# Kernel optimization log

Measured on AMD Instinct MI355X. Metric: run time of the kernel, lower is better.

Reference implementation:

```python
import jax, jax.numpy as jnp
import numpy as np

B, L, H, V = 8, 512, 256, 32000
ALPHA = 0.95  # EMA coefficient from __init__
LN_EPS = 1e-5
NORM_EPS = 1e-12  # F.normalize eps


def setup_inputs() -> dict:
    key = jax.random.key(0)
    ks = jax.random.split(key, 8)
    g = lambda k, shape, scale: (jax.random.normal(k, shape, jnp.float32) * scale)
    return {
        "seq": jax.random.randint(ks[0], (B, L), 0, V),
        "embed": g(ks[1], (V, H), 0.02),
        "W1": g(ks[2], (H, 2 * H), 1.0 / np.sqrt(H)),
        "b1": jnp.zeros((2 * H,), jnp.float32),
        "W2": g(ks[3], (2 * H, H), 1.0 / np.sqrt(2 * H)),
        "b2": jnp.zeros((H,), jnp.float32),
        "gamma": jnp.ones((H,), jnp.float32),
        "beta": jnp.zeros((H,), jnp.float32),
        "Wrp": g(ks[4], (H, H), 1.0 / np.sqrt(H)),
        "brp": jnp.zeros((H,), jnp.float32),
        "Wout": g(ks[5], (H, V), 1.0 / np.sqrt(H)),
        "bout": jnp.zeros((V,), jnp.float32),
    }


def _encoder(seq, embed, W1, b1, W2, b2, gamma, beta):
    h = embed[seq]  # [B, L, H]
    ff = jnp.maximum(h @ W1 + b1, 0.0) @ W2 + b2  # Linear-ReLU-Linear
    x = h + ff
    mu = x.mean(-1, keepdims=True)
    var = ((x - mu) ** 2).mean(-1, keepdims=True)
    return (x - mu) / jnp.sqrt(var + LN_EPS) * gamma + beta  # LayerNorm


def reference(seq, embed, W1, b1, W2, b2, gamma, beta, Wrp, brp, Wout, bout):
    h = _encoder(seq, embed, W1, b1, W2, b2, gamma, beta)  # [B, L, H]
    b, l, hd = h.shape
    keys = jnp.swapaxes(h[:, :-1, :], 0, 1)  # time-major [L-1, B, H]

    def step(M, k):
        kn = k / jnp.maximum(jnp.linalg.norm(k, axis=-1, keepdims=True), NORM_EPS)
        dv = k - jnp.einsum('bij,bj->bi', M, kn)  # delta: v - M k_hat
        M = M + (1.0 - ALPHA) * jnp.einsum('bi,bj->bij', dv, kn)  # rank-1 update
        return M, None

    M0 = jnp.zeros((b, hd, hd), h.dtype)
    M, _ = jax.lax.scan(step, M0, keys)  # sequential delta-rule recurrence
    m = jnp.einsum('bij,bj->bi', M, h[:, -1, :])  # read-out with last token
    return (m @ Wrp + brp) @ Wout + bout  # [B, V]
```

## Files before the change

kernel.cpp:

```cpp
#include <hip/hip_runtime.h>

constexpr int Bz  = 8;
constexpr int Lz  = 512;
constexpr int Hz  = 256;
constexpr int H2z = 512;
constexpr int Vz  = 32000;
constexpr int Mz  = Bz * Lz;
constexpr float CF = 0.05f;
constexpr int NB  = 16;

typedef __attribute__((ext_vector_type(8))) short bfrag8;
typedef __attribute__((ext_vector_type(4))) float f32x4v;
typedef __attribute__((ext_vector_type(4))) short s4v;

static __device__ __forceinline__ short f2bf(float f) {
  unsigned u = __builtin_bit_cast(unsigned, f);
  u += 0x7fffu + ((u >> 16) & 1u);
  return (short)(u >> 16);
}

static __device__ __forceinline__ void wcvt_tile(
    const float* __restrict__ src, short* __restrict__ dst,
    int K, int N, int n0, int k0, int tid)
{
  __shared__ float tile[64][68];
  const int rr = tid >> 4, c4 = (tid & 15) << 2;
#pragma unroll
  for (int q = 0; q < 4; ++q) {
    const int kr = rr + q * 16;
    *(float4*)&tile[kr][c4] = *(const float4*)(src + (long)(k0 + kr) * N + n0 + c4);
  }
  __syncthreads();
#pragma unroll
  for (int q = 0; q < 4; ++q) {
    const int nr = rr + q * 16;
    s4v o = { f2bf(tile[c4 + 0][nr]), f2bf(tile[c4 + 1][nr]),
              f2bf(tile[c4 + 2][nr]), f2bf(tile[c4 + 3][nr]) };
    *(s4v*)(dst + (long)(n0 + nr) * K + k0 + c4) = o;
  }
}

__global__ __launch_bounds__(256) void k_wcvt2(
    const float* __restrict__ W1, const float* __restrict__ W2,
    short* __restrict__ Wt1, short* __restrict__ Wt2)
{
  const int bx = blockIdx.x, tid = threadIdx.x;
  if (bx < 32) {
    wcvt_tile(W1, Wt1, Hz, H2z, (bx & 7) * 64, (bx >> 3) * 64, tid);
  } else {
    const int b2 = bx - 32;
    wcvt_tile(W2, Wt2, H2z, Hz, (b2 & 3) * 64, (b2 >> 2) * 64, tid);
  }
}

__global__ __launch_bounds__(256) void k_mfma1(
    const int* __restrict__ seq, const float* __restrict__ embed,
    const short* __restrict__ Wt1, const float* __restrict__ b1,
    short* __restrict__ y1bf)
{
  __shared__ short As[64][32];
  __shared__ short Bs[64][32];
  const int tid = threadIdx.x;
  const int n0 = blockIdx.x * 64, m0 = blockIdx.y * 64;
  const int w = tid >> 6, l = tid & 63;
  const int srow = tid >> 2, skq = (tid & 3) << 3;
  const long abase = (long)seq[m0 + srow] * Hz;
  const f32x4v zero = {0.f, 0.f, 0.f, 0.f};
  f32x4v acc[4] = {zero, zero, zero, zero};
  for (int kc = 0; kc < Hz; kc += 32) {
    const float4 a0 = *(const float4*)(embed + abase + kc + skq);
    const float4 a1 = *(const float4*)(embed + abase + kc + skq + 4);
    const bfrag8 bvl = *(const bfrag8*)(Wt1 + (long)(n0 + srow) * Hz + kc + skq);
    __syncthreads();
    bfrag8 av = { f2bf(a0.x), f2bf(a0.y), f2bf(a0.z), f2bf(a0.w),
                  f2bf(a1.x), f2bf(a1.y), f2bf(a1.z), f2bf(a1.w) };
    *(bfrag8*)&As[srow][skq] = av;
    *(bfrag8*)&Bs[srow][skq] = bvl;
    __syncthreads();
    const bfrag8 a = *(const bfrag8*)&As[(w << 4) + (l & 15)][(l >> 4) << 3];
#pragma unroll
    for (int nn = 0; nn < 4; ++nn) {
      const bfrag8 bb = *(const bfrag8*)&Bs[(nn << 4) + (l & 15)][(l >> 4) << 3];
      acc[nn] = __builtin_amdgcn_mfma_f32_16x16x32_bf16(a, bb, acc[nn], 0, 0, 0);
    }
  }
  const int col0 = l & 15, quad = l >> 4;
#pragma unroll
  for (int nn = 0; nn < 4; ++nn) {
    const int col = n0 + (nn << 4) + col0;
    const float bias = b1[col];
#pragma unroll
    for (int i = 0; i < 4; ++i) {
      const int row = m0 + (w << 4) + (quad << 2) + i;
      y1bf[(long)row * H2z + col] = f2bf(fmaxf(acc[nn][i] + bias, 0.0f));
    }
  }
}

__global__ __launch_bounds__(256) void k_mfma2(
    const int* __restrict__ seq, const float* __restrict__ embed,
    const short* __restrict__ y1bf, const short* __restrict__ Wt2,
    const float* __restrict__ b2, float* __restrict__ x)
{
  __shared__ short As[64][32];
  __shared__ short Bs[64][32];
  const int tid = threadIdx.x;
  const int n0 = blockIdx.x * 64, m0 = blockIdx.y * 64;
  const int w = tid >> 6, l = tid & 63;
  const int srow = tid >> 2, skq = (tid & 3) << 3;
  const f32x4v zero = {0.f, 0.f, 0.f, 0.f};
  f32x4v acc[4] = {zero, zero, zero, zero};
  for (int kc = 0; kc < H2z; kc += 32) {
    __syncthreads();
    *(bfrag8*)&As[srow][skq] = *(const bfrag8*)(y1bf + (long)(m0 + srow) * H2z + kc + skq);
    *(bfrag8*)&Bs[srow][skq] = *(const bfrag8*)(Wt2 + (long)(n0 + srow) * H2z + kc + skq);
    __syncthreads();
    const bfrag8 a = *(const bfrag8*)&As[(w << 4) + (l & 15)][(l >> 4) << 3];
#pragma unroll
    for (int nn = 0; nn < 4; ++nn) {
      const bfrag8 bb = *(const bfrag8*)&Bs[(nn << 4) + (l & 15)][(l >> 4) << 3];
      acc[nn] = __builtin_amdgcn_mfma_f32_16x16x32_bf16(a, bb, acc[nn], 0, 0, 0);
    }
  }
  const int col0 = l & 15, quad = l >> 4;
#pragma unroll
  for (int i = 0; i < 4; ++i) {
    const int row = m0 + (w << 4) + (quad << 2) + i;
    const long ebase = (long)seq[row] * Hz;
#pragma unroll
    for (int nn = 0; nn < 4; ++nn) {
      const int col = n0 + (nn << 4) + col0;
      x[(long)row * Hz + col] = acc[nn][i] + b2[col] + embed[ebase + col];
    }
  }
}

__global__ __launch_bounds__(256) void k_ln(
    const float* __restrict__ x, const float* __restrict__ gamma,
    const float* __restrict__ beta, float* __restrict__ h,
    float* __restrict__ hn, short* __restrict__ Knb)
{
  const int lane = threadIdx.x & 63;
  const long row = (long)blockIdx.x * 4 + (threadIdx.x >> 6);
  const int b = (int)(row >> 9), t = (int)(row & 511);
  const int off = lane << 2;
  const float4 xv = *(const float4*)(x + row * Hz + off);
  float s  = xv.x + xv.y + xv.z + xv.w;
  float ss = xv.x * xv.x + xv.y * xv.y + xv.z * xv.z + xv.w * xv.w;
#pragma unroll
  for (int o = 32; o >= 1; o >>= 1) { s += __shfl_xor(s, o); ss += __shfl_xor(ss, o); }
  const float mu   = s * (1.0f / Hz);
  const float var  = ss * (1.0f / Hz) - mu * mu;
  const float rstd = rsqrtf(var + 1e-5f);
  const float4 gv = *(const float4*)(gamma + off);
  const float4 bv = *(const float4*)(beta + off);
  float4 hv;
  hv.x = (xv.x - mu) * rstd * gv.x + bv.x;
  hv.y = (xv.y - mu) * rstd * gv.y + bv.y;
  hv.z = (xv.z - mu) * rstd * gv.z + bv.z;
  hv.w = (xv.w - mu) * rstd * gv.w + bv.w;
  *(float4*)(h + row * Hz + off) = hv;
  float hs = hv.x * hv.x + hv.y * hv.y + hv.z * hv.z + hv.w * hv.w;
#pragma unroll
  for (int o = 32; o >= 1; o >>= 1) hs += __shfl_xor(hs, o);
  const float inv = 1.0f / fmaxf(sqrtf(hs), 1e-12f);
  float4 nv = {hv.x * inv, hv.y * inv, hv.z * inv, hv.w * inv};
  *(float4*)(hn + row * Hz + off) = nv;
  if (t < 511) {
    const int sidx = 510 - t;
    s4v o = { f2bf(nv.x), f2bf(nv.y), f2bf(nv.z), f2bf(nv.w) };
    *(s4v*)(Knb + ((long)b * 512 + sidx) * Hz + off) = o;
  } else {
    s4v z = {0, 0, 0, 0};
    *(s4v*)(Knb + ((long)b * 512 + 511) * Hz + off) = z;
  }
}

__global__ __launch_bounds__(256) void k_gramT(
    const short* __restrict__ Knb, float* __restrict__ G)
{
  const int nb = blockIdx.x, mb = blockIdx.y, b = blockIdx.z;
  if (nb > mb) return;
  __shared__ short As[64][32];
  __shared__ short Bs[64][32];
  const short* Kb = Knb + (long)b * 512 * Hz;
  const int tid = threadIdx.x;
  const int w = tid >> 6, l = tid & 63;
  const int srow = tid >> 2, skq = (tid & 3) << 3;
  const f32x4v zero = {0.f, 0.f, 0.f, 0.f};
  f32x4v acc[4] = {zero, zero, zero, zero};
  for (int kc = 0; kc < Hz; kc += 32) {
    __syncthreads();
    *(bfrag8*)&As[srow][skq] = *(const bfrag8*)(Kb + (long)(mb * 64 + srow) * Hz + kc + skq);
    *(bfrag8*)&Bs[srow][skq] = *(const bfrag8*)(Kb + (long)(nb * 64 + srow) * Hz + kc + skq);
    __syncthreads();
    const bfrag8 a = *(const bfrag8*)&As[(w << 4) + (l & 15)][(l >> 4) << 3];
#pragma unroll
    for (int nn = 0; nn < 4; ++nn) {
      const bfrag8 bb = *(const bfrag8*)&Bs[(nn << 4) + (l & 15)][(l >> 4) << 3];
      acc[nn] = __builtin_amdgcn_mfma_f32_16x16x32_bf16(a, bb, acc[nn], 0, 0, 0);
    }
  }
  const int col0 = l & 15, quad = l >> 4;
  float* Gb = G + (long)b * 512 * 512;
#pragma unroll
  for (int nn = 0; nn < 4; ++nn) {
    const int col = nb * 64 + (nn << 4) + col0;
#pragma unroll
    for (int i = 0; i < 4; ++i) {
      const int row = mb * 64 + (w << 4) + (quad << 2) + i;
      Gb[(long)row * 512 + col] = acc[nn][i];
    }
  }
}

__global__ __launch_bounds__(256) void k_winv(
    const float* __restrict__ G, float* __restrict__ Wsol)
{
  __shared__ float Gs[32][33];
  __shared__ float Ws[32][33];
  __shared__ float part[8][33];
  const int blk = blockIdx.x, b = blockIdx.y;
  const int tid = threadIdx.x;
  const float* Gb = G + (long)b * 512 * 512;
  const int s0 = blk << 5;
  {
    const int i = tid >> 3, j4 = (tid & 7) << 2;
    *(float4*)&Gs[i][j4] = *(const float4*)(Gb + (long)(s0 + i) * 512 + s0 + j4);
    const float4 z = {0.f, 0.f, 0.f, 0.f};
    *(float4*)&Ws[i][j4] = z;
  }
  __syncthreads();
  if (tid == 0) Ws[0][0] = 1.0f;
  __syncthreads();
  const int c = tid & 31, g = tid >> 5;
  for (int i = 1; i < 32; ++i) {
    float partial = 0.0f;
#pragma unroll
    for (int q = 0; q < 4; ++q) {
      const int j = g + (q << 3);
      if (j < i) partial = fmaf(Gs[i][j], Ws[j][c], partial);
    }
    part[g][c] = partial;
    __syncthreads();
    if (tid < 32) {
      const float sum = part[0][c] + part[1][c] + part[2][c] + part[3][c] +
                        part[4][c] + part[5][c] + part[6][c] + part[7][c];
      Ws[i][c] = ((i == c) ? 1.0f : 0.0f) - CF * sum;
    }
    __syncthreads();
  }
  {
    const int i = tid >> 3, j4 = (tid & 7) << 2;
    float* dst = Wsol + ((long)(b * NB + blk) << 10);
    *(float4*)(dst + i * 32 + j4) = *(const float4*)&Ws[i][j4];
  }
}

__global__ __launch_bounds__(256) void k_p(
    const float* __restrict__ h, const float* __restrict__ hn,
    float* __restrict__ p)
{
  __shared__ float qs[Hz];
  const int b = blockIdx.y, tid = threadIdx.x;
  qs[tid] = h[((long)b * Lz + 511) * Hz + tid];
  __syncthreads();
  const int s = blockIdx.x * 16 + (tid >> 4);
  const int ch = (tid & 15) << 4;
  float acc = 0.0f;
  if (s <= 510) {
    const float* src = hn + ((long)b * Lz + (510 - s)) * Hz + ch;
#pragma unroll
    for (int q = 0; q < 4; ++q) {
      const float4 v = *(const float4*)(src + 4 * q);
      acc += v.x * qs[ch + 4 * q] + v.y * qs[ch + 4 * q + 1] +
             v.z * qs[ch + 4 * q + 2] + v.w * qs[ch + 4 * q + 3];
    }
  }
#pragma unroll
  for (int o = 8; o >= 1; o >>= 1) acc += __shfl_xor(acc, o);
  if ((tid & 15) == 0) p[(long)b * 512 + s] = acc;
}

__global__ __launch_bounds__(256) void k_solve(
    const float* __restrict__ G, const float* __restrict__ p,
    const float* __restrict__ Wsol, float* __restrict__ d_all)
{
  __shared__ float ds[512];
  __shared__ float part[32][9];
  __shared__ float rhs[32];
  const int b = blockIdx.x, tid = threadIdx.x;
  const int i = tid >> 3, g = tid & 7;
  const float* Gb = G + (long)b * 512 * 512;
  const float* pb = p + (long)b * 512;

  for (int blk = 0; blk < NB; ++blk) {
    float acc0 = 0.0f, acc1 = 0.0f;
    const float* grow = Gb + (long)(blk * 32 + i) * 512 + (g << 2);
    int bp = 0;
    for (; bp + 1 < blk; bp += 2) {
      const float4 g0 = *(const float4*)(grow + bp * 32);
      const float4 g1 = *(const float4*)(grow + bp * 32 + 32);
      const int j0 = bp * 32 + (g << 2), j1 = j0 + 32;
      acc0 += g0.x * ds[j0] + g0.y * ds[j0 + 1] + g0.z * ds[j0 + 2] + g0.w * ds[j0 + 3];
      acc1 += g1.x * ds[j1] + g1.y * ds[j1 + 1] + g1.z * ds[j1 + 2] + g1.w * ds[j1 + 3];
    }
    if (bp < blk) {
      const float4 gv = *(const float4*)(grow + bp * 32);
      const int j = bp * 32 + (g << 2);
      acc0 += gv.x * ds[j] + gv.y * ds[j + 1] + gv.z * ds[j + 2] + gv.w * ds[j + 3];
    }
    part[i][g] = acc0 + acc1;
    __syncthreads();
    if (tid < 32) {
      float c = part[tid][0] + part[tid][1] + part[tid][2] + part[tid][3] +
                part[tid][4] + part[tid][5] + part[tid][6] + part[tid][7];
      rhs[tid] = pb[blk * 32 + tid] - CF * c;
    }
    __syncthreads();
    const float* wrow = Wsol + ((long)(b * NB + blk) << 10) + i * 32 + (g << 2);
    const float4 wv = *(const float4*)wrow;
    const int k0 = g << 2;
    part[i][g] = wv.x * rhs[k0] + wv.y * rhs[k0 + 1] +
                 wv.z * rhs[k0 + 2] + wv.w * rhs[k0 + 3];
    __syncthreads();
    if (tid < 32) {
      float dv = part[tid][0] + part[tid][1] + part[tid][2] + part[tid][3] +
                 part[tid][4] + part[tid][5] + part[tid][6] + part[tid][7];
      if (blk == NB - 1 && tid == 31) dv = 0.0f;
      ds[blk * 32 + tid] = dv;
      d_all[(long)b * 512 + blk * 32 + tid] = dv;
    }
    __syncthreads();
  }
}

__global__ __launch_bounds__(256) void k_mrp(
    const float* __restrict__ h, const float* __restrict__ d_all,
    float* __restrict__ part)
{
  const int c = blockIdx.x, b = blockIdx.y, tid = threadIdx.x;
  const float* hb = h + (long)b * Lz * Hz;
  const float* db = d_all + ((long)b << 9);
  const int t0 = c * 16;
  const int t1 = (t0 + 16 < 511) ? t0 + 16 : 511;
  float acc = 0.0f;
#pragma unroll 4
  for (int t = t0; t < t1; ++t)
    acc = fmaf(db[510 - t], hb[(long)t * Hz + tid], acc);
  part[((long)b * 32 + c) * Hz + tid] = acc;
}

__global__ __launch_bounds__(256) void k_mr2(
    const float* __restrict__ part, const float* __restrict__ Wrp,
    const float* __restrict__ brp, float* __restrict__ r)
{
  __shared__ float ms[Hz];
  const int b = blockIdx.x, tid = threadIdx.x;
  float acc = 0.0f;
#pragma unroll
  for (int c = 0; c < 32; ++c) acc += part[((long)b * 32 + c) * Hz + tid];
  ms[tid] = CF * acc;
  __syncthreads();
  float racc = 0.0f;
#pragma unroll 8
  for (int e = 0; e < Hz; ++e)
    racc = fmaf(ms[e], Wrp[(long)e * Hz + tid], racc);
  r[b * Hz + tid] = racc + brp[tid];
}

__global__ __launch_bounds__(256) void k_outproj(
    const float* __restrict__ r, const float* __restrict__ Wout,
    const float* __restrict__ bout, float* __restrict__ out)
{
  __shared__ float rs[8 * Hz];
  __shared__ float part[4][8][64];
  const int tid = threadIdx.x, w = tid >> 6, lane = tid & 63;
  ((float4*)rs)[tid * 2 + 0] = ((const float4*)r)[tid * 2 + 0];
  ((float4*)rs)[tid * 2 + 1] = ((const float4*)r)[tid * 2 + 1];
  __syncthreads();
  const int col = blockIdx.x * 64 + lane;
  float acc[8] = {};
  const int i0 = w << 6;
#pragma unroll 8
  for (int ii = 0; ii < 64; ++ii) {
    const int i = i0 + ii;
    const float wv = Wout[(long)i * Vz + col];
#pragma unroll
    for (int bb = 0; bb < 8; ++bb) acc[bb] = fmaf(rs[bb * Hz + i], wv, acc[bb]);
  }
#pragma unroll
  for (int bb = 0; bb < 8; ++bb) part[w][bb][lane] = acc[bb];
  __syncthreads();
  const float bo = bout[col];
  float s0 = part[0][w][lane] + part[1][w][lane] + part[2][w][lane] + part[3][w][lane];
  out[(long)w * Vz + col] = s0 + bo;
  const int w4 = w + 4;
  float s1 = part[0][w4][lane] + part[1][w4][lane] + part[2][w4][lane] + part[3][w4][lane];
  out[(long)w4 * Vz + col] = s1 + bo;
}

extern "C" void kernel_launch(void* const* d_in, const int* in_sizes, int n_in,
                              void* d_out, int out_size, void* d_ws, size_t ws_size,
                              hipStream_t stream)
{
  const int*   seq   = (const int*)  d_in[0];
  const float* embed = (const float*)d_in[1];
  const float* W1    = (const float*)d_in[2];
  const float* b1    = (const float*)d_in[3];
  const float* W2    = (const float*)d_in[4];
  const float* b2    = (const float*)d_in[5];
  const float* gamma = (const float*)d_in[6];
  const float* beta  = (const float*)d_in[7];
  const float* Wrp   = (const float*)d_in[8];
  const float* brp   = (const float*)d_in[9];
  const float* Wout  = (const float*)d_in[10];
  const float* bout  = (const float*)d_in[11];
  float* out = (float*)d_out;

  char* ws = (char*)d_ws;
  const size_t MB = 1024u * 1024u;
  short* y1bf = (short*)(ws);
  float* xb   = (float*)(ws + 4 * MB);
  float* Gf   = (float*)(ws);
  float* hb   = (float*)(ws + 8 * MB);
  float* hnb  = (float*)(ws + 12 * MB);
  short* Knb  = (short*)(ws + 16 * MB);
  short* Wt1  = (short*)(ws + 18 * MB);
  short* Wt2  = (short*)(ws + 18 * MB + 256 * 1024);
  float* Wsol = (float*)(ws + 18 * MB + 512 * 1024);
  float* pbuf = (float*)(ws + 19 * MB);
  float* dall = (float*)(ws + 19 * MB + 16 * 1024);
  float* prt  = (float*)(ws + 19 * MB + 32 * 1024);
  float* rb   = (float*)(ws + 19 * MB + 288 * 1024);

  k_wcvt2<<<64, 256, 0, stream>>>(W1, W2, Wt1, Wt2);
  k_mfma1<<<dim3(H2z / 64, Mz / 64), 256, 0, stream>>>(seq, embed, Wt1, b1, y1bf);
  k_mfma2<<<dim3(Hz / 64, Mz / 64), 256, 0, stream>>>(seq, embed, y1bf, Wt2, b2, xb);
  k_ln<<<Mz / 4, 256, 0, stream>>>(xb, gamma, beta, hb, hnb, Knb);
  k_gramT<<<dim3(8, 8, Bz), 256, 0, stream>>>(Knb, Gf);
  k_winv<<<dim3(NB, Bz), 256, 0, stream>>>(Gf, Wsol);
  k_p<<<dim3(32, Bz), 256, 0, stream>>>(hb, hnb, pbuf);
  k_solve<<<Bz, 256, 0, stream>>>(Gf, pbuf, Wsol, dall);
  k_mrp<<<dim3(32, Bz), 256, 0, stream>>>(hb, dall, prt);
  k_mr2<<<Bz, 256, 0, stream>>>(prt, Wrp, brp, rb);
  k_outproj<<<Vz / 64, 256, 0, stream>>>(rb, Wout, bout, out);
}
```

Baseline: 205.3 us.

## Fuse diagonal-block inverse into gram kernel and merge solve tail into one kernel

The 32x32 diagonal-block triangular inverse now runs inside the gram kernel's diagonal tiles, working on the accumulator values still held there, so the separate k_winv launch and its reread of G go away. The p projection, blocked forward solve, M readout and Wrp projection are merged into a single 1024-thread per-batch kernel, with the Wsol blocks staged in shared memory. This removes five launches and their intermediate global round-trips. In exchange, the tail runs on only 8 blocks, the inverse is serial per column in registers, and the larger block means more threads wait at each barrier.

```diff
diff --git a/kernel.cpp b/kernel.cpp
--- a/kernel.cpp
+++ b/kernel.cpp
@@ -177,12 +177,14 @@
 }
 
 __global__ __launch_bounds__(256) void k_gramT(
-    const short* __restrict__ Knb, float* __restrict__ G)
+    const short* __restrict__ Knb, float* __restrict__ G,
+    float* __restrict__ Wsol)
 {
   const int nb = blockIdx.x, mb = blockIdx.y, b = blockIdx.z;
   if (nb > mb) return;
   __shared__ short As[64][32];
   __shared__ short Bs[64][32];
+  __shared__ float Gs2[2][32][33];
   const short* Kb = Knb + (long)b * 512 * Hz;
   const int tid = threadIdx.x;
   const int w = tid >> 6, l = tid & 63;
@@ -212,161 +214,135 @@
       Gb[(long)row * 512 + col] = acc[nn][i];
     }
   }
-}
-
-__global__ __launch_bounds__(256) void k_winv(
-    const float* __restrict__ G, float* __restrict__ Wsol)
-{
-  __shared__ float Gs[32][33];
-  __shared__ float Ws[32][33];
-  __shared__ float part[8][33];
-  const int blk = blockIdx.x, b = blockIdx.y;
-  const int tid = threadIdx.x;
-  const float* Gb = G + (long)b * 512 * 512;
-  const int s0 = blk << 5;
+  if (mb != nb) return;
+#pragma unroll
+  for (int nn = 0; nn < 4; ++nn) {
+    const int lc = (nn << 4) + col0;
+#pragma unroll
+    for (int i = 0; i < 4; ++i) {
+      const int lr = (w << 4) + (quad << 2) + i;
+      if ((lr >> 5) == (lc >> 5)) Gs2[lr >> 5][lr & 31][lc & 31] = acc[nn][i];
+    }
+  }
+  __syncthreads();
+  if (w < 2 && l < 32) {
+    const int c = l;
+    float wv[32];
+    wv[0] = (c == 0) ? 1.0f : 0.0f;
+#pragma unroll
+    for (int i = 1; i < 32; ++i) {
+      float sum = 0.0f;
+#pragma unroll
+      for (int j = 0; j < i; ++j) sum = fmaf(Gs2[w][i][j], wv[j], sum);
+      wv[i] = ((i == c) ? 1.0f : 0.0f) - CF * sum;
+    }
+    const int blk = mb * 2 + w;
+    float* dst = Wsol + ((long)(b * NB + blk) << 10) + c;
+#pragma unroll
+    for (int i = 0; i < 32; ++i) dst[i * 32] = wv[i];
+  }
+}
+
+__global__ __launch_bounds__(1024) void k_tail(
+    const float* __restrict__ h, const float* __restrict__ hn,
+    const float* __restrict__ G, const float* __restrict__ Wsol,
+    const float* __restrict__ Wrp, const float* __restrict__ brp,
+    float* __restrict__ r)
+{
+  __shared__ float Wl[16][32][32];
+  __shared__ float qs[256];
+  __shared__ float ps[512];
+  __shared__ float ds[512];
+  __shared__ float part[32][33];
+  __shared__ float rhs[32];
+  __shared__ float pm[4][256];
+  __shared__ float ms[256];
+  const int b = blockIdx.x, tid = threadIdx.x;
+  const float* hb  = h  + (long)b * Lz * Hz;
+  const float* hnb = hn + (long)b * Lz * Hz;
+  const float* Gb  = G + (long)b * 512 * 512;
+
+  if (tid < 256) qs[tid] = hb[511 * Hz + tid];
   {
-    const int i = tid >> 3, j4 = (tid & 7) << 2;
-    *(float4*)&Gs[i][j4] = *(const float4*)(Gb + (long)(s0 + i) * 512 + s0 + j4);
-    const float4 z = {0.f, 0.f, 0.f, 0.f};
-    *(float4*)&Ws[i][j4] = z;
-  }
-  __syncthreads();
-  if (tid == 0) Ws[0][0] = 1.0f;
-  __syncthreads();
-  const int c = tid & 31, g = tid >> 5;
-  for (int i = 1; i < 32; ++i) {
-    float partial = 0.0f;
-#pragma unroll
-    for (int q = 0; q < 4; ++q) {
-      const int j = g + (q << 3);
-      if (j < i) partial = fmaf(Gs[i][j], Ws[j][c], partial);
-    }
-    part[g][c] = partial;
+    const float4* src = (const float4*)(Wsol + ((long)(b * NB) << 10));
+    float4* dst = (float4*)&Wl[0][0][0];
+#pragma unroll
+    for (int q = 0; q < 4; ++q) dst[tid + q * 1024] = src[tid + q * 1024];
+  }
+  __syncthreads();
+
+  {
+    const int s = tid >> 1, hf = tid & 1;
+    float acc = 0.0f;
+    if (s < 511) {
+      const float* src = hnb + (long)(510 - s) * Hz + hf * 128;
+#pragma unroll
+      for (int q = 0; q < 32; ++q) {
+        const float4 v = *(const float4*)(src + 4 * q);
+        const int e = hf * 128 + 4 * q;
+        acc += v.x * qs[e] + v.y * qs[e + 1] + v.z * qs[e + 2] + v.w * qs[e + 3];
+      }
+    }
+    acc += __shfl_xor(acc, 1);
+    if (hf == 0) ps[s] = acc;
+  }
+  __syncthreads();
+
+  const int si = tid >> 5, sg = tid & 31;
+  for (int blk = 0; blk < NB; ++blk) {
+    float acc = 0.0f;
+    const float* grow = Gb + (long)(blk * 32 + si) * 512;
+    const int nq = (blk + 3) >> 2;
+    for (int q = 0; q < nq; ++q) {
+      const int c = (sg << 2) + (q << 7);
+      if (c < blk * 32) {
+        const float4 gv = *(const float4*)(grow + c);
+        acc += gv.x * ds[c] + gv.y * ds[c + 1] + gv.z * ds[c + 2] + gv.w * ds[c + 3];
+      }
+    }
+    part[si][sg] = acc;
     __syncthreads();
     if (tid < 32) {
-      const float sum = part[0][c] + part[1][c] + part[2][c] + part[3][c] +
-                        part[4][c] + part[5][c] + part[6][c] + part[7][c];
-      Ws[i][c] = ((i == c) ? 1.0f : 0.0f) - CF * sum;
-    }
-    __syncthreads();
-  }
-  {
-    const int i = tid >> 3, j4 = (tid & 7) << 2;
-    float* dst = Wsol + ((long)(b * NB + blk) << 10);
-    *(float4*)(dst + i * 32 + j4) = *(const float4*)&Ws[i][j4];
-  }
-}
-
-__global__ __launch_bounds__(256) void k_p(
-    const float* __restrict__ h, const float* __restrict__ hn,
-    float* __restrict__ p)
-{
-  __shared__ float qs[Hz];
-  const int b = blockIdx.y, tid = threadIdx.x;
-  qs[tid] = h[((long)b * Lz + 511) * Hz + tid];
-  __syncthreads();
-  const int s = blockIdx.x * 16 + (tid >> 4);
-  const int ch = (tid & 15) << 4;
-  float acc = 0.0f;
-  if (s <= 510) {
-    const float* src = hn + ((long)b * Lz + (510 - s)) * Hz + ch;
-#pragma unroll
-    for (int q = 0; q < 4; ++q) {
-      const float4 v = *(const float4*)(src + 4 * q);
-      acc += v.x * qs[ch + 4 * q] + v.y * qs[ch + 4 * q + 1] +
-             v.z * qs[ch + 4 * q + 2] + v.w * qs[ch + 4 * q + 3];
-    }
-  }
-#pragma unroll
-  for (int o = 8; o >= 1; o >>= 1) acc += __shfl_xor(acc, o);
-  if ((tid & 15) == 0) p[(long)b * 512 + s] = acc;
-}
-
-__global__ __launch_bounds__(256) void k_solve(
-    const float* __restrict__ G, const float* __restrict__ p,
-    const float* __restrict__ Wsol, float* __restrict__ d_all)
-{
-  __shared__ float ds[512];
-  __shared__ float part[32][9];
-  __shared__ float rhs[32];
-  const int b = blockIdx.x, tid = threadIdx.x;
-  const int i = tid >> 3, g = tid & 7;
-  const float* Gb = G + (long)b * 512 * 512;
-  const float* pb = p + (long)b * 512;
-
-  for (int blk = 0; blk < NB; ++blk) {
-    float acc0 = 0.0f, acc1 = 0.0f;
-    const float* grow = Gb + (long)(blk * 32 + i) * 512 + (g << 2);
-    int bp = 0;
-    for (; bp + 1 < blk; bp += 2) {
-      const float4 g0 = *(const float4*)(grow + bp * 32);
-      const float4 g1 = *(const float4*)(grow + bp * 32 + 32);
-      const int j0 = bp * 32 + (g << 2), j1 = j0 + 32;
-      acc0 += g0.x * ds[j0] + g0.y * ds[j0 + 1] + g0.z * ds[j0 + 2] + g0.w * ds[j0 + 3];
-      acc1 += g1.x * ds[j1] + g1.y * ds[j1 + 1] + g1.z * ds[j1 + 2] + g1.w * ds[j1 + 3];
-    }
-    if (bp < blk) {
-      const float4 gv = *(const float4*)(grow + bp * 32);
-      const int j = bp * 32 + (g << 2);
-      acc0 += gv.x * ds[j] + gv.y * ds[j + 1] + gv.z * ds[j + 2] + gv.w * ds[j + 3];
-    }
-    part[i][g] = acc0 + acc1;
+      float s8 = 0.0f;
+#pragma unroll
+      for (int k = 0; k < 32; ++k) s8 += part[tid][k];
+      rhs[tid] = ps[blk * 32 + tid] - CF * s8;
+    }
+    __syncthreads();
+    part[si][sg] = Wl[blk][si][sg] * rhs[sg];
     __syncthreads();
     if (tid < 32) {
-      float c = part[tid][0] + part[tid][1] + part[tid][2] + part[tid][3] +
-                part[tid][4] + part[tid][5] + part[tid][6] + part[tid][7];
-      rhs[tid] = pb[blk * 32 + tid] - CF * c;
-    }
-    __syncthreads();
-    const float* wrow = Wsol + ((long)(b * NB + blk) << 10) + i * 32 + (g << 2);
-    const float4 wv = *(const float4*)wrow;
-    const int k0 = g << 2;
-    part[i][g] = wv.x * rhs[k0] + wv.y * rhs[k0 + 1] +
-                 wv.z * rhs[k0 + 2] + wv.w * rhs[k0 + 3];
-    __syncthreads();
-    if (tid < 32) {
-      float dv = part[tid][0] + part[tid][1] + part[tid][2] + part[tid][3] +
-                 part[tid][4] + part[tid][5] + part[tid][6] + part[tid][7];
+      float dv = 0.0f;
+#pragma unroll
+      for (int k = 0; k < 32; ++k) dv += part[tid][k];
       if (blk == NB - 1 && tid == 31) dv = 0.0f;
       ds[blk * 32 + tid] = dv;
-      d_all[(long)b * 512 + blk * 32 + tid] = dv;
-    }
-    __syncthreads();
-  }
-}
-
-__global__ __launch_bounds__(256) void k_mrp(
-    const float* __restrict__ h, const float* __restrict__ d_all,
-    float* __restrict__ part)
-{
-  const int c = blockIdx.x, b = blockIdx.y, tid = threadIdx.x;
-  const float* hb = h + (long)b * Lz * Hz;
-  const float* db = d_all + ((long)b << 9);
-  const int t0 = c * 16;
-  const int t1 = (t0 + 16 < 511) ? t0 + 16 : 511;
-  float acc = 0.0f;
-#pragma unroll 4
-  for (int t = t0; t < t1; ++t)
-    acc = fmaf(db[510 - t], hb[(long)t * Hz + tid], acc);
-  part[((long)b * 32 + c) * Hz + tid] = acc;
-}
-
-__global__ __launch_bounds__(256) void k_mr2(
-    const float* __restrict__ part, const float* __restrict__ Wrp,
-    const float* __restrict__ brp, float* __restrict__ r)
-{
-  __shared__ float ms[Hz];
-  const int b = blockIdx.x, tid = threadIdx.x;
-  float acc = 0.0f;
-#pragma unroll
-  for (int c = 0; c < 32; ++c) acc += part[((long)b * 32 + c) * Hz + tid];
-  ms[tid] = CF * acc;
-  __syncthreads();
-  float racc = 0.0f;
+    }
+    __syncthreads();
+  }
+
+  {
+    const int c = tid & 255, q4 = tid >> 8;
+    float acc = 0.0f;
+    const int t0 = q4 << 7;
+    for (int t = t0; t < t0 + 128; ++t)
+      if (t < 511) acc = fmaf(ds[510 - t], hb[(long)t * Hz + c], acc);
+    pm[q4][c] = acc;
+  }
+  __syncthreads();
+  if (tid < 256) ms[tid] = CF * (pm[0][tid] + pm[1][tid] + pm[2][tid] + pm[3][tid]);
+  __syncthreads();
+  {
+    const int c = tid & 255, eq = tid >> 8;
+    float acc = 0.0f;
 #pragma unroll 8
-  for (int e = 0; e < Hz; ++e)
-    racc = fmaf(ms[e], Wrp[(long)e * Hz + tid], racc);
-  r[b * Hz + tid] = racc + brp[tid];
+    for (int e = eq * 64; e < eq * 64 + 64; ++e)
+      acc = fmaf(ms[e], Wrp[(long)e * Hz + c], acc);
+    pm[eq][c] = acc;
+  }
+  __syncthreads();
+  if (tid < 256)
+    r[b * Hz + tid] = pm[0][tid] + pm[1][tid] + pm[2][tid] + pm[3][tid] + brp[tid];
 }
 
 __global__ __launch_bounds__(256) void k_outproj(
@@ -429,20 +405,13 @@
   short* Wt1  = (short*)(ws + 18 * MB);
   short* Wt2  = (short*)(ws + 18 * MB + 256 * 1024);
   float* Wsol = (float*)(ws + 18 * MB + 512 * 1024);
-  float* pbuf = (float*)(ws + 19 * MB);
-  float* dall = (float*)(ws + 19 * MB + 16 * 1024);
-  float* prt  = (float*)(ws + 19 * MB + 32 * 1024);
-  float* rb   = (float*)(ws + 19 * MB + 288 * 1024);
+  float* rb   = (float*)(ws + 19 * MB);
 
   k_wcvt2<<<64, 256, 0, stream>>>(W1, W2, Wt1, Wt2);
   k_mfma1<<<dim3(H2z / 64, Mz / 64), 256, 0, stream>>>(seq, embed, Wt1, b1, y1bf);
   k_mfma2<<<dim3(Hz / 64, Mz / 64), 256, 0, stream>>>(seq, embed, y1bf, Wt2, b2, xb);
   k_ln<<<Mz / 4, 256, 0, stream>>>(xb, gamma, beta, hb, hnb, Knb);
-  k_gramT<<<dim3(8, 8, Bz), 256, 0, stream>>>(Knb, Gf);
-  k_winv<<<dim3(NB, Bz), 256, 0, stream>>>(Gf, Wsol);
-  k_p<<<dim3(32, Bz), 256, 0, stream>>>(hb, hnb, pbuf);
-  k_solve<<<Bz, 256, 0, stream>>>(Gf, pbuf, Wsol, dall);
-  k_mrp<<<dim3(32, Bz), 256, 0, stream>>>(hb, dall, prt);
-  k_mr2<<<Bz, 256, 0, stream>>>(prt, Wrp, brp, rb);
+  k_gramT<<<dim3(8, 8, Bz), 256, 0, stream>>>(Knb, Gf, Wsol);
+  k_tail<<<Bz, 1024, 0, stream>>>(hb, hnb, Gf, Wsol, Wrp, brp, rb);
   k_outproj<<<Vz / 64, 256, 0, stream>>>(rb, Wout, bout, out);
 }
```

Result: no change. 206.7 us (+0.7%).

## Fuse diagonal-block triangular inverse into Gram kernel and vectorize readout partials

Applied to the files above, without the earlier changes.

The 32x32 diagonal-block triangular inversion that k_winv ran as a separate launch is now done at the end of k_gramT by the diagonal-tile blocks, using the accumulators already held in registers. Each inversion is a per-thread serial forward substitution instead of a barrier-synchronised loop. This drops one kernel launch and the reload of G from global memory, but the diagonal blocks now finish late and carry a register-heavy serial tail. k_mrp is also rewritten to use float4 loads with the time steps split across wavefronts, reduced through shared memory.

```diff
diff --git a/kernel.cpp b/kernel.cpp
--- a/kernel.cpp
+++ b/kernel.cpp
@@ -177,12 +177,14 @@
 }
 
 __global__ __launch_bounds__(256) void k_gramT(
-    const short* __restrict__ Knb, float* __restrict__ G)
+    const short* __restrict__ Knb, float* __restrict__ G,
+    float* __restrict__ Wsol)
 {
   const int nb = blockIdx.x, mb = blockIdx.y, b = blockIdx.z;
   if (nb > mb) return;
   __shared__ short As[64][32];
   __shared__ short Bs[64][32];
+  __shared__ float Gs2[2][32][33];
   const short* Kb = Knb + (long)b * 512 * Hz;
   const int tid = threadIdx.x;
   const int w = tid >> 6, l = tid & 63;
@@ -212,48 +214,32 @@
       Gb[(long)row * 512 + col] = acc[nn][i];
     }
   }
-}
-
-__global__ __launch_bounds__(256) void k_winv(
-    const float* __restrict__ G, float* __restrict__ Wsol)
-{
-  __shared__ float Gs[32][33];
-  __shared__ float Ws[32][33];
-  __shared__ float part[8][33];
-  const int blk = blockIdx.x, b = blockIdx.y;
-  const int tid = threadIdx.x;
-  const float* Gb = G + (long)b * 512 * 512;
-  const int s0 = blk << 5;
-  {
-    const int i = tid >> 3, j4 = (tid & 7) << 2;
-    *(float4*)&Gs[i][j4] = *(const float4*)(Gb + (long)(s0 + i) * 512 + s0 + j4);
-    const float4 z = {0.f, 0.f, 0.f, 0.f};
-    *(float4*)&Ws[i][j4] = z;
-  }
-  __syncthreads();
-  if (tid == 0) Ws[0][0] = 1.0f;
-  __syncthreads();
-  const int c = tid & 31, g = tid >> 5;
-  for (int i = 1; i < 32; ++i) {
-    float partial = 0.0f;
-#pragma unroll
-    for (int q = 0; q < 4; ++q) {
-      const int j = g + (q << 3);
-      if (j < i) partial = fmaf(Gs[i][j], Ws[j][c], partial);
-    }
-    part[g][c] = partial;
-    __syncthreads();
-    if (tid < 32) {
-      const float sum = part[0][c] + part[1][c] + part[2][c] + part[3][c] +
-                        part[4][c] + part[5][c] + part[6][c] + part[7][c];
-      Ws[i][c] = ((i == c) ? 1.0f : 0.0f) - CF * sum;
-    }
-    __syncthreads();
-  }
-  {
-    const int i = tid >> 3, j4 = (tid & 7) << 2;
-    float* dst = Wsol + ((long)(b * NB + blk) << 10);
-    *(float4*)(dst + i * 32 + j4) = *(const float4*)&Ws[i][j4];
+  if (mb != nb) return;
+#pragma unroll
+  for (int nn = 0; nn < 4; ++nn) {
+    const int lc = (nn << 4) + col0;
+#pragma unroll
+    for (int i = 0; i < 4; ++i) {
+      const int lr = (w << 4) + (quad << 2) + i;
+      if ((lr >> 5) == (lc >> 5)) Gs2[lr >> 5][lr & 31][lc & 31] = acc[nn][i];
+    }
+  }
+  __syncthreads();
+  if (w < 2 && l < 32) {
+    const int c = l;
+    float wv[32];
+    wv[0] = (c == 0) ? 1.0f : 0.0f;
+#pragma unroll
+    for (int i = 1; i < 32; ++i) {
+      float sum = 0.0f;
+#pragma unroll
+      for (int j = 0; j < i; ++j) sum = fmaf(Gs2[w][i][j], wv[j], sum);
+      wv[i] = ((i == c) ? 1.0f : 0.0f) - CF * sum;
+    }
+    const int blk = mb * 2 + w;
+    float* dst = Wsol + ((long)(b * NB + blk) << 10) + c;
+#pragma unroll
+    for (int i = 0; i < 32; ++i) dst[i * 32] = wv[i];
   }
 }
 
@@ -339,16 +325,30 @@
     const float* __restrict__ h, const float* __restrict__ d_all,
     float* __restrict__ part)
 {
+  __shared__ float acc_s[4][Hz];
   const int c = blockIdx.x, b = blockIdx.y, tid = threadIdx.x;
+  const int w = tid >> 6, lane = tid & 63;
   const float* hb = h + (long)b * Lz * Hz;
   const float* db = d_all + ((long)b << 9);
   const int t0 = c * 16;
-  const int t1 = (t0 + 16 < 511) ? t0 + 16 : 511;
-  float acc = 0.0f;
-#pragma unroll 4
-  for (int t = t0; t < t1; ++t)
-    acc = fmaf(db[510 - t], hb[(long)t * Hz + tid], acc);
-  part[((long)b * 32 + c) * Hz + tid] = acc;
+  const int off = lane << 2;
+  float4 acc = {0.f, 0.f, 0.f, 0.f};
+#pragma unroll
+  for (int q = 0; q < 4; ++q) {
+    const int t = t0 + (q << 2) + w;
+    if (t < 511) {
+      const float dv = db[510 - t];
+      const float4 hv = *(const float4*)(hb + (long)t * Hz + off);
+      acc.x = fmaf(dv, hv.x, acc.x); acc.y = fmaf(dv, hv.y, acc.y);
+      acc.z = fmaf(dv, hv.z, acc.z); acc.w = fmaf(dv, hv.w, acc.w);
+    }
+  }
+  *(float4*)&acc_s[w][off] = acc;
+  __syncthreads();
+  if (tid < Hz) {
+    part[((long)b * 32 + c) * Hz + tid] =
+        acc_s[0][tid] + acc_s[1][tid] + acc_s[2][tid] + acc_s[3][tid];
+  }
 }
 
 __global__ __launch_bounds__(256) void k_mr2(
@@ -438,8 +438,7 @@
   k_mfma1<<<dim3(H2z / 64, Mz / 64), 256, 0, stream>>>(seq, embed, Wt1, b1, y1bf);
   k_mfma2<<<dim3(Hz / 64, Mz / 64), 256, 0, stream>>>(seq, embed, y1bf, Wt2, b2, xb);
   k_ln<<<Mz / 4, 256, 0, stream>>>(xb, gamma, beta, hb, hnb, Knb);
-  k_gramT<<<dim3(8, 8, Bz), 256, 0, stream>>>(Knb, Gf);
-  k_winv<<<dim3(NB, Bz), 256, 0, stream>>>(Gf, Wsol);
+  k_gramT<<<dim3(8, 8, Bz), 256, 0, stream>>>(Knb, Gf, Wsol);
   k_p<<<dim3(32, Bz), 256, 0, stream>>>(hb, hnb, pbuf);
   k_solve<<<Bz, 256, 0, stream>>>(Gf, pbuf, Wsol, dall);
   k_mrp<<<dim3(32, Bz), 256, 0, stream>>>(hb, dall, prt);
```

Result: faster. 200.7 us (-2.2%).
